# Optimization experiments

Hardware: AMD Instinct MI355X
Metric: run time of the kernel (lower is better)

## Reference

```python
import jax, jax.numpy as jnp
from jax import lax
import numpy as np

IMGSIZE = (360, 640)  # (H, W)
SIGMA = 71.0
LEVEL = 5
FACTOR = 2.0

_k1 = np.array([1., 4., 6., 4., 1.], dtype=np.float32) / 16.0
K5 = np.outer(_k1, _k1)  # 5x5 binomial (Gaussian) pyramid kernel


def _blur(x, scale=1.0):
    # x: (B,C,H,W); depthwise 5x5 Gaussian blur with reflect padding
    C = x.shape[1]
    xp = jnp.pad(x, ((0, 0), (0, 0), (2, 2), (2, 2)), mode='reflect')
    k = jnp.broadcast_to(jnp.asarray(K5 * scale, x.dtype), (C, 1, 5, 5))
    return lax.conv_general_dilated(xp, k, (1, 1), 'VALID',
                                    feature_group_count=C,
                                    dimension_numbers=('NCHW', 'OIHW', 'NCHW'))


def pyrdown(x):
    # OpenCV-style pyrDown: blur then drop every other row/col -> ceil(H/2), ceil(W/2)
    return _blur(x)[:, :, ::2, ::2]


def pyrup(x):
    # OpenCV-style pyrUp: zero-insertion upsample then blur with 4*kernel
    B, C, H, W = x.shape
    up = jnp.zeros((B, C, 2 * H, 2 * W), x.dtype).at[:, :, ::2, ::2].set(x)
    return _blur(up, scale=4.0)


def resize_nearest(x, h, w):
    # matches torch F.interpolate(mode='nearest'): src = floor(dst * in/out)
    H, W = x.shape[-2], x.shape[-1]
    ri = jnp.arange(h) * H // h
    ci = jnp.arange(w) * W // w
    return x[..., ri[:, None], ci[None, :]]


def _create_filter(height, width, sigma):
    s = 2.0 * sigma * sigma
    xc = int(round(width * 0.5))
    yc = int(round(height * 0.5))
    ex = jnp.arange(-xc, width - xc - 1, dtype=jnp.float32)   # (W-1,)
    ey = jnp.arange(-yc, height - yc - 1, dtype=jnp.float32)  # (H-1,)
    d = ex[:, None] ** 2 + ey[None, :] ** 2                   # (W-1, H-1)
    g = jnp.exp(-d / s)
    return (g / g.max()).T                                    # (H-1, W-1)


def _pyramid_filters():
    f = _create_filter(int(FACTOR * IMGSIZE[0]), int(FACTOR * IMGSIZE[1]), SIGMA)
    filters = [f]
    for _ in range(LEVEL):
        filters.append(pyrdown(filters[-1][None, None])[0, 0])
    return filters


def setup_inputs():
    key = jax.random.key(0)
    k1, k2 = jax.random.split(key)
    B, C = 32, 3
    H, W = IMGSIZE
    images = jax.random.normal(k1, (B, C, H, W), jnp.float32)
    u = jax.random.uniform(k2, (B, 2), jnp.float32)
    # fixations are (x, y) pixel coordinates inside the image
    fixations = u * jnp.array([W - 1.0, H - 1.0], jnp.float32)
    return {"images": images, "fixations": fixations}


def reference(images, fixations):
    filters = _pyramid_filters()
    # Laplacian pyramid construction
    pyr, cur = [], images
    up = images
    for _ in range(LEVEL):
        dn = pyrdown(cur)
        up = resize_nearest(pyrup(dn), cur.shape[2], cur.shape[3])
        pyr.append(cur - up)
        cur = dn
    fovea = up  # smallest level, upsampled back (im_smallest)
    for i in range(LEVEL - 1, -1, -1):
        f = filters[i]
        fh, fw = f.shape
        ih, iw = pyr[i].shape[2], pyr[i].shape[3]
        fix = fixations / (2.0 ** i)
        # rect = filter_size/2 - fix, truncated to int (same as torch .to(int64))
        x1 = (fw / 2.0 - fix[:, 0]).astype(jnp.int32)
        y1 = (fh / 2.0 - fix[:, 1]).astype(jnp.int32)
        # per-sample dynamic crop of size (ih, iw); crop size == target size so
        # the original's F.interpolate on the crop is the identity
        crop = jax.vmap(lambda yy, xx: lax.dynamic_slice(f, (yy, xx), (ih, iw)))(y1, x1)
        filtered = pyr[i] * crop[:, None, :, :]
        if i != LEVEL - 1:
            fovea = resize_nearest(pyrup(fovea), ih, iw)
        fovea = fovea + filtered
    return fovea
```

## Files before the change

kernel.cpp:

```cpp
#include <hip/hip_runtime.h>
#include <cstddef>


static __device__ __forceinline__ int refl(int e, int n) {
  if (e < 0) e = -e;
  if (e >= n) e = 2 * n - 2 - e;
  return e;
}

static __device__ __forceinline__ int mapi(int i, int n) {
  return i < 0 ? -i : (i >= n ? n - 1 : i);
}

static __device__ __forceinline__ float4 loadu4(const float* p) {
  float4 v; __builtin_memcpy(&v, p, sizeof(float4)); return v;
}

static __device__ void filt_build(float* pool, float* __restrict__ fyg,
                                  float* __restrict__ fxg) {
  float* sy = pool;
  float* sx = pool + 1394;
  const int oy[5] = {0, 719, 1079, 1259, 1349};
  const int ny[5] = {719, 360, 180, 90, 45};
  const int ox[5] = {0, 1279, 1919, 2239, 2399};
  const int nx[5] = {1279, 640, 320, 160, 80};
  int tid = threadIdx.y * 64 + threadIdx.x;
  for (int i = tid; i < 719; i += 256) {
    float d = (float)(i - 360); sy[i] = expf(-d * d / 10082.0f);
  }
  for (int i = tid; i < 1279; i += 256) {
    float d = (float)(i - 640); sx[i] = expf(-d * d / 10082.0f);
  }
  __syncthreads();
  const float k0 = 0.0625f, k1 = 0.25f, k2 = 0.375f;
#pragma unroll
  for (int l = 1; l < 5; ++l) {
    const float* py = sy + oy[l - 1]; float* qy = sy + oy[l];
    int n = ny[l - 1];
    for (int i = tid; i < ny[l]; i += 256) {
      qy[i] = k0 * (py[refl(2 * i - 2, n)] + py[refl(2 * i + 2, n)]) +
              k1 * (py[refl(2 * i - 1, n)] + py[refl(2 * i + 1, n)]) +
              k2 * py[2 * i];
    }
    const float* px = sx + ox[l - 1]; float* qx = sx + ox[l];
    int m = nx[l - 1];
    for (int i = tid; i < nx[l]; i += 256) {
      qx[i] = k0 * (px[refl(2 * i - 2, m)] + px[refl(2 * i + 2, m)]) +
              k1 * (px[refl(2 * i - 1, m)] + px[refl(2 * i + 1, m)]) +
              k2 * px[2 * i];
    }
    __syncthreads();
  }
  for (int i = tid; i < 1394; i += 256) fyg[i] = sy[i];
  for (int i = tid; i < 2479; i += 256) fxg[i] = sx[i];
}

__global__ __launch_bounds__(256) void pyrdown_lds_k(
    const float* __restrict__ src, float* __restrict__ dst,
    int H, int W, int oH, int oW, int NP,
    float* __restrict__ fyo, float* __restrict__ fxo) {
  __shared__ float pool[35 * 68 * 2];
  int tx = threadIdx.x;
  int ty = threadIdx.y;
  int p  = blockIdx.z;
  if (p >= NP) {
    if (blockIdx.x == 0 && blockIdx.y == 0 && fyo) filt_build(pool, fyo, fxo);
    return;
  }
  float* te = pool;
  float* to_ = pool + 35 * 68;
  int x0 = blockIdx.x * 64;
  int Yb = blockIdx.y;
  const float* s = src + (size_t)p * H * W;
  float* d = dst + (size_t)p * oH * oW;

  int cols = min(64, oW - x0);
  int nq   = (cols + 4) >> 1;
  int gr0  = 32 * Yb - 2;
  int gc0  = 2 * x0 - 4;
  int tid  = ty * 64 + tx;

  auto loadq = [&](int r, int m) -> float4 {
    int gy = refl(gr0 + r, H);
    const float* row = s + (size_t)gy * W;
    int gc = gc0 + 4 * m;
    if (gc >= 0 && gc + 3 < W) return *(const float4*)(row + gc);
    float4 v;
    v.x = row[refl(gc, W)];
    v.y = row[refl(gc + 1, W)];
    v.z = row[refl(gc + 2, W)];
    v.w = row[refl(gc + 3, W)];
    return v;
  };
  auto putq = [&](int r, int m, float4 v) {
    *(float2*)&te[r * 68 + 2 * m]  = make_float2(v.x, v.z);
    *(float2*)&to_[r * 68 + 2 * m] = make_float2(v.y, v.w);
  };

  if (nq == 34) {
    int r0 = tid / 34,          m0 = tid - 34 * r0;
    int q1 = tid + 256;  int r1 = q1 / 34, m1 = q1 - 34 * r1;
    int q2 = tid + 512;  int r2 = q2 / 34, m2 = q2 - 34 * r2;
    int q3 = tid + 768;  int r3 = q3 / 34, m3 = q3 - 34 * r3;
    int q4 = tid + 1024; int r4 = q4 / 34, m4 = q4 - 34 * r4;
    bool g4 = (q4 < 1190);
    float4 v0 = loadq(r0, m0);
    float4 v1 = loadq(r1, m1);
    float4 v2 = loadq(r2, m2);
    float4 v3 = loadq(r3, m3);
    float4 v4;
    if (g4) v4 = loadq(r4, m4);
    putq(r0, m0, v0);
    putq(r1, m1, v1);
    putq(r2, m2, v2);
    putq(r3, m3, v3);
    if (g4) putq(r4, m4, v4);
  } else {
    float4 v[9];
#pragma unroll
    for (int i = 0; i < 9; ++i) {
      int r = ty + 4 * i;
      if (r < 35 && tx < nq) v[i] = loadq(r, tx);
    }
#pragma unroll
    for (int i = 0; i < 9; ++i) {
      int r = ty + 4 * i;
      if (r < 35 && tx < nq) putq(r, tx, v[i]);
    }
  }
  __syncthreads();

  int x = x0 + tx;
  int nPairs = (oH + 1) >> 1;
  int Yp0 = 8 * Yb + 2 * ty;
  if (x < oW && Yp0 < nPairs) {
    const float k0 = 0.0625f, k1 = 0.25f, k2 = 0.375f;
    float h[11];
    int rbase = 8 * ty;
#pragma unroll
    for (int a = 0; a < 11; ++a) {
      int r = rbase + a;
      float e0 = te[r * 68 + tx + 1], e2 = te[r * 68 + tx + 2],
            e4 = te[r * 68 + tx + 3];
      float e1 = to_[r * 68 + tx + 1], e3 = to_[r * 68 + tx + 2];
      h[a] = k0 * (e0 + e4) + k1 * (e1 + e3) + k2 * e2;
    }
    float o0 = k0 * (h[0] + h[4])  + k1 * (h[1] + h[3])  + k2 * h[2];
    float o1 = k0 * (h[2] + h[6])  + k1 * (h[3] + h[5])  + k2 * h[4];
    float o2 = k0 * (h[4] + h[8])  + k1 * (h[5] + h[7])  + k2 * h[6];
    float o3 = k0 * (h[6] + h[10]) + k1 * (h[7] + h[9])  + k2 * h[8];
    int oy0 = 2 * Yp0;
    float* drow = d + (size_t)oy0 * oW + x;
    drow[0] = o0;
    if (oy0 + 1 < oH) drow[(size_t)oW] = o1;
    if (oy0 + 2 < oH) drow[(size_t)2 * oW] = o2;
    if (oy0 + 3 < oH) drow[(size_t)3 * oW] = o3;
  }
}

static __device__ __forceinline__ float pyrdown_at(const float* c, int H, int W,
                                                   int y, int x) {
  const float k0 = 0.0625f, k1 = 0.25f, k2 = 0.375f;
  int c0 = refl(2 * x - 2, W), c1 = refl(2 * x - 1, W), c2 = 2 * x,
      c3 = refl(2 * x + 1, W), c4 = refl(2 * x + 2, W);
  float h[5];
#pragma unroll
  for (int r = 0; r < 5; ++r) {
    int gy = refl(2 * y - 2 + r, H);
    const float* row = c + gy * W;
    h[r] = k0 * (row[c0] + row[c4]) + k1 * (row[c1] + row[c3]) + k2 * row[c2];
  }
  return k0 * (h[0] + h[4]) + k1 * (h[1] + h[3]) + k2 * h[2];
}

static __device__ __forceinline__ float pyrup_at(const float* c, int Hc, int Wc,
                                                 int y, int x) {
  const float w0 = 0.125f, w1 = 0.75f;
  int yc = y >> 1, xc = x >> 1;
  if (y & 1) {
    int yb = (yc == Hc - 1) ? Hc - 1 : yc + 1;
    const float* ra = c + yc * Wc;
    const float* rb = c + yb * Wc;
    if (x & 1) {
      int xb = (xc == Wc - 1) ? Wc - 1 : xc + 1;
      return 0.25f * (ra[xc] + ra[xb] + rb[xc] + rb[xb]);
    } else {
      int xm = (xc == 0) ? 1 : xc - 1, xp = (xc == Wc - 1) ? Wc - 1 : xc + 1;
      float a = w1 * ra[xc] + w0 * (ra[xm] + ra[xp]);
      float b = w1 * rb[xc] + w0 * (rb[xm] + rb[xp]);
      return 0.5f * (a + b);
    }
  } else {
    int ym = (yc == 0) ? 1 : yc - 1, yp = (yc == Hc - 1) ? Hc - 1 : yc + 1;
    const float* rm = c + ym * Wc;
    const float* rc = c + yc * Wc;
    const float* rp = c + yp * Wc;
    if (x & 1) {
      int xb = (xc == Wc - 1) ? Wc - 1 : xc + 1;
      float a = 0.5f * (rm[xc] + rm[xb]);
      float b = 0.5f * (rc[xc] + rc[xb]);
      float e = 0.5f * (rp[xc] + rp[xb]);
      return w1 * b + w0 * (a + e);
    } else {
      int xm = (xc == 0) ? 1 : xc - 1, xp = (xc == Wc - 1) ? Wc - 1 : xc + 1;
      float a = w1 * rm[xc] + w0 * (rm[xm] + rm[xp]);
      float b = w1 * rc[xc] + w0 * (rc[xm] + rc[xp]);
      float e = w1 * rp[xc] + w0 * (rp[xm] + rp[xp]);
      return w1 * b + w0 * (a + e);
    }
  }
}

static __device__ __forceinline__ float pyrup_flat(
    const float* t, int pitch, int yo, int xo, int y, int x) {
  const float w0 = 0.125f, w1 = 0.75f;
  int ys = (y >> 1) - yo, xs = (x >> 1) - xo;
  const float* rc = t + ys * pitch + xs;
  float h0, h1, h2;
  if (x & 1) {
    h1 = 0.5f * (rc[0] + rc[1]);
    h2 = 0.5f * (rc[pitch] + rc[pitch + 1]);
    if (y & 1) return 0.5f * (h1 + h2);
    h0 = 0.5f * (rc[-pitch] + rc[-pitch + 1]);
    return w1 * h1 + w0 * (h0 + h2);
  } else {
    h1 = w1 * rc[0] + w0 * (rc[-1] + rc[1]);
    h2 = w1 * rc[pitch] + w0 * (rc[pitch - 1] + rc[pitch + 1]);
    if (y & 1) return 0.5f * (h1 + h2);
    h0 = w1 * rc[-pitch] + w0 * (rc[-pitch - 1] + rc[-pitch + 1]);
    return w1 * h1 + w0 * (h0 + h2);
  }
}

__global__ __launch_bounds__(256) void tail_k(
    const float* __restrict__ dn3, const float* __restrict__ fix,
    const float* __restrict__ fy3, const float* __restrict__ fx3,
    const float* __restrict__ fy4, const float* __restrict__ fx4,
    float* __restrict__ fv3) {
  __shared__ float c3[45 * 80];
  __shared__ float c4[23 * 40];
  __shared__ float c5[12 * 20];
  __shared__ float g4[23 * 40];
  int p = blockIdx.x;
  int tid = threadIdx.x;
  const float* src = dn3 + (size_t)p * 3600;
  for (int i = tid; i < 900; i += 256)
    ((float4*)c3)[i] = ((const float4*)src)[i];
  __syncthreads();
  for (int i = tid; i < 23 * 40; i += 256) {
    int y = i / 40, x = i - 40 * y;
    c4[i] = pyrdown_at(c3, 45, 80, y, x);
  }
  __syncthreads();
  for (int i = tid; i < 12 * 20; i += 256) {
    int y = i / 20, x = i - 20 * y;
    c5[i] = pyrdown_at(c4, 23, 40, y, x);
  }
  __syncthreads();
  int b = p / 3;
  float fxv = fix[2 * b + 0], fyv = fix[2 * b + 1];
  {
    int x1 = (int)(40.0f - fxv * 0.0625f);
    int y1 = (int)(22.5f - fyv * 0.0625f);
    for (int i = tid; i < 23 * 40; i += 256) {
      int y = i / 40, x = i - 40 * y;
      float u = pyrup_at(c5, 12, 20, y, x);
      g4[i] = u + (c4[i] - u) * (fy4[y1 + y] * fx4[x1 + x]);
    }
  }
  __syncthreads();
  {
    int x1 = (int)(80.0f - fxv * 0.125f);
    int y1 = (int)(45.0f - fyv * 0.125f);
    float* dst = fv3 + (size_t)p * 3600;
    for (int i = tid; i < 45 * 80; i += 256) {
      int y = i / 80, x = i - 80 * y;
      float uf = pyrup_at(g4, 23, 40, y, x);
      float ud = pyrup_at(c4, 23, 40, y, x);
      dst[i] = uf + (c3[i] - ud) * (fy3[y1 + y] * fx3[x1 + x]);
    }
  }
}

__global__ __launch_bounds__(256) void recon_fused_k(
    const float* __restrict__ images, const float* __restrict__ dn1,
    const float* __restrict__ dn2, const float* __restrict__ dn3,
    const float* __restrict__ fv3g, const float* __restrict__ fyg,
    const float* __restrict__ fxg, const float* __restrict__ fix,
    float* __restrict__ out) {
  __shared__ float fv1t[10 * 67];
  __shared__ float dn1t[10 * 67];
  __shared__ float fv2t[7 * 35];
  __shared__ float dn2t[7 * 35];
  __shared__ float fv3t[5 * 19];
  __shared__ float dn3t[5 * 19];
  const int bx = blockIdx.x, by = blockIdx.y, p = blockIdx.z;
  const int tid = threadIdx.x;
  const int R1o = 8 * by - 1, C1o = 64 * bx - 1;
  const int R2o = 4 * by - 1, C2o = 32 * bx - 1;
  const int R3o = 2 * by - 1, C3o = 16 * bx - 1;
  const float* d1p = dn1 + (size_t)p * 57600;
  const float* d2p = dn2 + (size_t)p * 14400;
  const float* d3p = dn3 + (size_t)p * 3600;
  const float* f3p = fv3g + (size_t)p * 3600;

  for (int s = tid; s < 660; s += 256) {
    int r = s / 66, c = s - 66 * r;
    int gy = mapi(R1o + r, 180), gx = mapi(C1o + c, 320);
    dn1t[r * 67 + c] = d1p[gy * 320 + gx];
  }
  if (tid < 245) {
    int r = tid / 35, c = tid - 35 * r;
    int gy = mapi(R2o + r, 90), gx = mapi(C2o + c, 160);
    dn2t[tid] = d2p[gy * 160 + gx];
  }
  if (tid < 95) {
    int r = tid / 19, c = tid - 19 * r;
    int gy = mapi(R3o + r, 45), gx = mapi(C3o + c, 80);
    dn3t[tid] = d3p[gy * 80 + gx];
    fv3t[tid] = f3p[gy * 80 + gx];
  }
  __syncthreads();

  int b = p / 3;
  float fxv = fix[2 * b + 0], fyv = fix[2 * b + 1];
  int y1_2 = (int)(90.0f - fyv * 0.25f), x1_2 = (int)(160.0f - fxv * 0.25f);
  int y1_1 = (int)(180.0f - fyv * 0.5f), x1_1 = (int)(320.0f - fxv * 0.5f);
  int y1_0 = (int)(359.5f - fyv),        x1_0 = (int)(639.5f - fxv);
  const float* fy2 = fyg + 1079; const float* fx2 = fxg + 1919;
  const float* fy1 = fyg + 719;  const float* fx1 = fxg + 1279;

  if (tid < 245) {
    int r = tid / 35, c = tid - 35 * r;
    int gy = mapi(R2o + r, 90), gx = mapi(C2o + c, 160);
    float uf = pyrup_flat(fv3t, 19, R3o, C3o, gy, gx);
    float ud = pyrup_flat(dn3t, 19, R3o, C3o, gy, gx);
    fv2t[tid] = uf + (dn2t[tid] - ud) * (fy2[y1_2 + gy] * fx2[x1_2 + gx]);
  }
  __syncthreads();

  for (int s = tid; s < 660; s += 256) {
    int r = s / 66, c = s - 66 * r;
    int gy = mapi(R1o + r, 180), gx = mapi(C1o + c, 320);
    float uf = pyrup_flat(fv2t, 35, R2o, C2o, gy, gx);
    float ud = pyrup_flat(dn2t, 35, R2o, C2o, gy, gx);
    fv1t[r * 67 + c] =
        uf + (dn1t[r * 67 + c] - ud) * (fy1[y1_1 + gy] * fx1[x1_1 + gx]);
  }
  __syncthreads();

  int trow = tid >> 5;
  int tk   = tid & 31;
  int Y = 8 * by + trow;
  if (Y >= 180) return;
  int c0 = 64 * bx + 2 * tk;
  const float* dbase = dn1t + trow * 67 + 2 * tk;
  const float* ebase = fv1t + trow * 67 + 2 * tk;
  float dm[3], da[3], db[3], dq[3], em[3], ea[3], eb[3], eq[3];
#pragma unroll
  for (int r = 0; r < 3; ++r) {
    const float* q = dbase + r * 67;
    dm[r] = q[0]; da[r] = q[1]; db[r] = q[2]; dq[r] = q[3];
    const float* e = ebase + r * 67;
    em[r] = e[0]; ea[r] = e[1]; eb[r] = e[2]; eq[r] = e[3];
  }

  const float w0 = 0.125f, w1 = 0.75f;
  float heA[3], hoA[3], heB[3], hoB[3];
#pragma unroll
  for (int r = 0; r < 3; ++r) {
    heA[r] = w1 * da[r] + w0 * (dm[r] + db[r]);
    hoA[r] = 0.5f * (da[r] + db[r]);
    heB[r] = w1 * db[r] + w0 * (da[r] + dq[r]);
    hoB[r] = 0.5f * (db[r] + dq[r]);
  }
  float u00 = w1 * heA[1] + w0 * (heA[0] + heA[2]);
  float u01 = w1 * hoA[1] + w0 * (hoA[0] + hoA[2]);
  float u02 = w1 * heB[1] + w0 * (heB[0] + heB[2]);
  float u03 = w1 * hoB[1] + w0 * (hoB[0] + hoB[2]);
  float u10 = 0.5f * (heA[1] + heA[2]);
  float u11 = 0.5f * (hoA[1] + hoA[2]);
  float u12 = 0.5f * (heB[1] + heB[2]);
  float u13 = 0.5f * (hoB[1] + hoB[2]);

  float geA[3], goA[3], geB[3], goB[3];
#pragma unroll
  for (int r = 0; r < 3; ++r) {
    geA[r] = w1 * ea[r] + w0 * (em[r] + eb[r]);
    goA[r] = 0.5f * (ea[r] + eb[r]);
    geB[r] = w1 * eb[r] + w0 * (ea[r] + eq[r]);
    goB[r] = 0.5f * (eb[r] + eq[r]);
  }
  float f00 = w1 * geA[1] + w0 * (geA[0] + geA[2]);
  float f01 = w1 * goA[1] + w0 * (goA[0] + goA[2]);
  float f02 = w1 * geB[1] + w0 * (geB[0] + geB[2]);
  float f03 = w1 * goB[1] + w0 * (goB[0] + goB[2]);
  float f10 = 0.5f * (geA[1] + geA[2]);
  float f11 = 0.5f * (goA[1] + goA[2]);
  float f12 = 0.5f * (geB[1] + geB[2]);
  float f13 = 0.5f * (goB[1] + goB[2]);

  int oy = 2 * Y, ox = 2 * c0;
  const float* crow = images + (size_t)p * 230400 + (size_t)oy * 640 + ox;
  float* orow = out + (size_t)p * 230400 + (size_t)oy * 640 + ox;
  float fyA = fyg[y1_0 + oy], fyB = fyg[y1_0 + oy + 1];
  float4 fxq = loadu4(fxg + (x1_0 + ox));

  float4 cv = *(const float4*)crow;
  float4 r0v;
  r0v.x = f00 + (cv.x - u00) * (fyA * fxq.x);
  r0v.y = f01 + (cv.y - u01) * (fyA * fxq.y);
  r0v.z = f02 + (cv.z - u02) * (fyA * fxq.z);
  r0v.w = f03 + (cv.w - u03) * (fyA * fxq.w);
  *(float4*)orow = r0v;
  float4 cv1 = *(const float4*)(crow + 640);
  float4 r1v;
  r1v.x = f10 + (cv1.x - u10) * (fyB * fxq.x);
  r1v.y = f11 + (cv1.y - u11) * (fyB * fxq.y);
  r1v.z = f12 + (cv1.z - u12) * (fyB * fxq.z);
  r1v.w = f13 + (cv1.w - u13) * (fyB * fxq.w);
  *(float4*)(orow + 640) = r1v;
}

extern "C" void kernel_launch(void* const* d_in, const int* in_sizes, int n_in,
                              void* d_out, int out_size, void* d_ws, size_t ws_size,
                              hipStream_t stream) {
  const float* images = (const float*)d_in[0];
  const float* fix    = (const float*)d_in[1];
  float* out = (float*)d_out;
  float* ws  = (float*)d_ws;

  const int P = 96;

  size_t off = 0;
  auto alloc = [&](size_t n) { float* p = ws + off; off += (n + 3) & ~(size_t)3; return p; };
  float* fyg = alloc(1394);
  float* fxg = alloc(2479);
  float* dn1 = alloc((size_t)P * 180 * 320);
  float* dn2 = alloc((size_t)P * 90 * 160);
  float* dn3 = alloc((size_t)P * 45 * 80);
  float* fv3 = alloc((size_t)P * 45 * 80);
  if (ws_size < off * sizeof(float)) return;

  dim3 blk(64, 4, 1);
  auto pgrd = [](int oW, int oH, int p) {
    int nPairs = (oH + 1) / 2;
    return dim3((unsigned)((oW + 63) / 64), (unsigned)((nPairs + 7) / 8), (unsigned)p);
  };

  pyrdown_lds_k<<<pgrd(320, 180, P + 1), blk, 0, stream>>>(
      images, dn1, 360, 640, 180, 320, P, fyg, fxg);
  pyrdown_lds_k<<<pgrd(160, 90, P), blk, 0, stream>>>(
      dn1, dn2, 180, 320, 90, 160, P, nullptr, nullptr);
  pyrdown_lds_k<<<pgrd(80, 45, P), blk, 0, stream>>>(
      dn2, dn3, 90, 160, 45, 80, P, nullptr, nullptr);

  tail_k<<<dim3(P), dim3(256), 0, stream>>>(
      dn3, fix, fyg + 1259, fxg + 2239, fyg + 1349, fxg + 2399, fv3);

  recon_fused_k<<<dim3(5, 23, P), dim3(256), 0, stream>>>(
      images, dn1, dn2, dn3, fv3, fyg, fxg, fix, out);
}
```

Before: 233.3 us.

## Compute pyramid reconstruction per coarse cell producing 2x2 outputs, drop halo duplication

The fused reconstruction kernel now stages only the in-range tile rows and columns instead of mirrored halos. Each thread computes the shared horizontal and vertical pyrUp partial sums once per coarse cell and emits all four fine outputs, rather than recomputing the full stencil per output pixel. Border reflection moves into index arithmetic at use time. This removes redundant separable-filter arithmetic and per-pixel parity branching in the level-3 to level-2 and level-2 to level-1 stages, at the cost of more complex index bookkeeping and bounds checks.

```diff
diff --git a/kernel.cpp b/kernel.cpp
--- a/kernel.cpp
+++ b/kernel.cpp
@@ -6,10 +6,6 @@
   if (e < 0) e = -e;
   if (e >= n) e = 2 * n - 2 - e;
   return e;
-}
-
-static __device__ __forceinline__ int mapi(int i, int n) {
-  return i < 0 ? -i : (i >= n ? n - 1 : i);
 }
 
 static __device__ __forceinline__ float4 loadu4(const float* p) {
@@ -211,27 +207,6 @@
   }
 }
 
-static __device__ __forceinline__ float pyrup_flat(
-    const float* t, int pitch, int yo, int xo, int y, int x) {
-  const float w0 = 0.125f, w1 = 0.75f;
-  int ys = (y >> 1) - yo, xs = (x >> 1) - xo;
-  const float* rc = t + ys * pitch + xs;
-  float h0, h1, h2;
-  if (x & 1) {
-    h1 = 0.5f * (rc[0] + rc[1]);
-    h2 = 0.5f * (rc[pitch] + rc[pitch + 1]);
-    if (y & 1) return 0.5f * (h1 + h2);
-    h0 = 0.5f * (rc[-pitch] + rc[-pitch + 1]);
-    return w1 * h1 + w0 * (h0 + h2);
-  } else {
-    h1 = w1 * rc[0] + w0 * (rc[-1] + rc[1]);
-    h2 = w1 * rc[pitch] + w0 * (rc[pitch - 1] + rc[pitch + 1]);
-    if (y & 1) return 0.5f * (h1 + h2);
-    h0 = w1 * rc[-pitch] + w0 * (rc[-pitch - 1] + rc[-pitch + 1]);
-    return w1 * h1 + w0 * (h0 + h2);
-  }
-}
-
 __global__ __launch_bounds__(256) void tail_k(
     const float* __restrict__ dn3, const float* __restrict__ fix,
     const float* __restrict__ fy3, const float* __restrict__ fx3,
@@ -288,37 +263,48 @@
     const float* __restrict__ fv3g, const float* __restrict__ fyg,
     const float* __restrict__ fxg, const float* __restrict__ fix,
     float* __restrict__ out) {
-  __shared__ float fv1t[10 * 67];
-  __shared__ float dn1t[10 * 67];
-  __shared__ float fv2t[7 * 35];
-  __shared__ float dn2t[7 * 35];
-  __shared__ float fv3t[5 * 19];
-  __shared__ float dn3t[5 * 19];
+  __shared__ float dn1t[670], fv1t[670];
+  __shared__ float dn2t[296], fv2t[296];
+  __shared__ float dn3t[126], fv3t[126];
   const int bx = blockIdx.x, by = blockIdx.y, p = blockIdx.z;
   const int tid = threadIdx.x;
-  const int R1o = 8 * by - 1, C1o = 64 * bx - 1;
-  const int R2o = 4 * by - 1, C2o = 32 * bx - 1;
-  const int R3o = 2 * by - 1, C3o = 16 * bx - 1;
+
+  const int R1r = max(8 * by - 1, 0),  R1hi = min(8 * by + 8, 179);
+  const int C1r = max(64 * bx - 1, 0), C1hi = min(64 * bx + 64, 319);
+  const int n1r = R1hi - R1r + 1, n1c = C1hi - C1r + 1;
+  const int yc_lo = R1r >> 1, yc_hi = R1hi >> 1;
+  const int xc_lo = C1r >> 1, xc_hi = C1hi >> 1;
+  const int R2r = max(yc_lo - 1, 0),  R2hi = min(yc_hi + 1, 89);
+  const int C2r = max(xc_lo - 1, 0),  C2hi = min(xc_hi + 1, 159);
+  const int n2r = R2hi - R2r + 1, n2c = C2hi - C2r + 1;
+  const int yc3_lo = R2r >> 1, yc3_hi = R2hi >> 1;
+  const int xc3_lo = C2r >> 1, xc3_hi = C2hi >> 1;
+  const int R3r = max(yc3_lo - 1, 0), R3hi = min(yc3_hi + 1, 44);
+  const int C3r = max(xc3_lo - 1, 0), C3hi = min(xc3_hi + 1, 79);
+  const int n3r = R3hi - R3r + 1, n3c = C3hi - C3r + 1;
+
   const float* d1p = dn1 + (size_t)p * 57600;
   const float* d2p = dn2 + (size_t)p * 14400;
   const float* d3p = dn3 + (size_t)p * 3600;
   const float* f3p = fv3g + (size_t)p * 3600;
 
-  for (int s = tid; s < 660; s += 256) {
-    int r = s / 66, c = s - 66 * r;
-    int gy = mapi(R1o + r, 180), gx = mapi(C1o + c, 320);
-    dn1t[r * 67 + c] = d1p[gy * 320 + gx];
-  }
-  if (tid < 245) {
-    int r = tid / 35, c = tid - 35 * r;
-    int gy = mapi(R2o + r, 90), gx = mapi(C2o + c, 160);
-    dn2t[tid] = d2p[gy * 160 + gx];
-  }
-  if (tid < 95) {
-    int r = tid / 19, c = tid - 19 * r;
-    int gy = mapi(R3o + r, 45), gx = mapi(C3o + c, 80);
-    dn3t[tid] = d3p[gy * 80 + gx];
-    fv3t[tid] = f3p[gy * 80 + gx];
+  for (int s = tid; s < 670; s += 256) {
+    int r = s / 67, c = s - 67 * r;
+    if (r < n1r && c < n1c)
+      dn1t[s] = d1p[(R1r + r) * 320 + (C1r + c)];
+  }
+  for (int s = tid; s < 296; s += 256) {
+    int r = s / 37, c = s - 37 * r;
+    if (r < n2r && c < n2c)
+      dn2t[s] = d2p[(R2r + r) * 160 + (C2r + c)];
+  }
+  if (tid < 126) {
+    int r = tid / 21, c = tid - 21 * r;
+    if (r < n3r && c < n3c) {
+      int o = (R3r + r) * 80 + (C3r + c);
+      dn3t[tid] = d3p[o];
+      fv3t[tid] = f3p[o];
+    }
   }
   __syncthreads();
 
@@ -329,23 +315,99 @@
   int y1_0 = (int)(359.5f - fyv),        x1_0 = (int)(639.5f - fxv);
   const float* fy2 = fyg + 1079; const float* fx2 = fxg + 1919;
   const float* fy1 = fyg + 719;  const float* fx1 = fxg + 1279;
-
-  if (tid < 245) {
-    int r = tid / 35, c = tid - 35 * r;
-    int gy = mapi(R2o + r, 90), gx = mapi(C2o + c, 160);
-    float uf = pyrup_flat(fv3t, 19, R3o, C3o, gy, gx);
-    float ud = pyrup_flat(dn3t, 19, R3o, C3o, gy, gx);
-    fv2t[tid] = uf + (dn2t[tid] - ud) * (fy2[y1_2 + gy] * fx2[x1_2 + gx]);
-  }
-  __syncthreads();
-
-  for (int s = tid; s < 660; s += 256) {
-    int r = s / 66, c = s - 66 * r;
-    int gy = mapi(R1o + r, 180), gx = mapi(C1o + c, 320);
-    float uf = pyrup_flat(fv2t, 35, R2o, C2o, gy, gx);
-    float ud = pyrup_flat(dn2t, 35, R2o, C2o, gy, gx);
-    fv1t[r * 67 + c] =
-        uf + (dn1t[r * 67 + c] - ud) * (fy1[y1_1 + gy] * fx1[x1_1 + gx]);
+  const float w0 = 0.125f, w1 = 0.75f;
+
+  {
+    int nx3 = xc3_hi - xc3_lo + 1;
+    int ncell = (yc3_hi - yc3_lo + 1) * nx3;
+    if (tid < ncell) {
+      int cy = tid / nx3;
+      int yc = yc3_lo + cy, xc = xc3_lo + (tid - cy * nx3);
+      int aa0 = ((yc == 0) ? 1 : yc - 1) - R3r;
+      int aa1 = yc - R3r;
+      int aa2 = ((yc == 44) ? 44 : yc + 1) - R3r;
+      int xm = ((xc == 0) ? 1 : xc - 1) - C3r;
+      int xq = xc - C3r;
+      int xp = ((xc == 79) ? 79 : xc + 1) - C3r;
+      int aa[3] = {aa0, aa1, aa2};
+      float heF[3], hoF[3], heD[3], hoD[3];
+#pragma unroll
+      for (int j = 0; j < 3; ++j) {
+        const float* rf = fv3t + aa[j] * 21;
+        float fm = rf[xm], fc = rf[xq], fp = rf[xp];
+        heF[j] = w1 * fc + w0 * (fm + fp);
+        hoF[j] = 0.5f * (fc + fp);
+        const float* rd = dn3t + aa[j] * 21;
+        float em = rd[xm], ec = rd[xq], ep = rd[xp];
+        heD[j] = w1 * ec + w0 * (em + ep);
+        hoD[j] = 0.5f * (ec + ep);
+      }
+      float uF[4] = {w1 * heF[1] + w0 * (heF[0] + heF[2]),
+                     w1 * hoF[1] + w0 * (hoF[0] + hoF[2]),
+                     0.5f * (heF[1] + heF[2]),
+                     0.5f * (hoF[1] + hoF[2])};
+      float uD[4] = {w1 * heD[1] + w0 * (heD[0] + heD[2]),
+                     w1 * hoD[1] + w0 * (hoD[0] + hoD[2]),
+                     0.5f * (heD[1] + heD[2]),
+                     0.5f * (hoD[1] + hoD[2])};
+      int y2 = 2 * yc, x2 = 2 * xc;
+#pragma unroll
+      for (int q = 0; q < 4; ++q) {
+        int y = y2 + (q >> 1), x = x2 + (q & 1);
+        if (y >= R2r && y <= R2hi && x >= C2r && x <= C2hi) {
+          int idx = (y - R2r) * 37 + (x - C2r);
+          float w = fy2[y1_2 + y] * fx2[x1_2 + x];
+          fv2t[idx] = uF[q] + (dn2t[idx] - uD[q]) * w;
+        }
+      }
+    }
+  }
+  __syncthreads();
+
+  {
+    int nx2 = xc_hi - xc_lo + 1;
+    int ncell = (yc_hi - yc_lo + 1) * nx2;
+    if (tid < ncell) {
+      int cy = tid / nx2;
+      int yc = yc_lo + cy, xc = xc_lo + (tid - cy * nx2);
+      int aa0 = ((yc == 0) ? 1 : yc - 1) - R2r;
+      int aa1 = yc - R2r;
+      int aa2 = ((yc == 89) ? 89 : yc + 1) - R2r;
+      int xm = ((xc == 0) ? 1 : xc - 1) - C2r;
+      int xq = xc - C2r;
+      int xp = ((xc == 159) ? 159 : xc + 1) - C2r;
+      int aa[3] = {aa0, aa1, aa2};
+      float heF[3], hoF[3], heD[3], hoD[3];
+#pragma unroll
+      for (int j = 0; j < 3; ++j) {
+        const float* rf = fv2t + aa[j] * 37;
+        float fm = rf[xm], fc = rf[xq], fp = rf[xp];
+        heF[j] = w1 * fc + w0 * (fm + fp);
+        hoF[j] = 0.5f * (fc + fp);
+        const float* rd = dn2t + aa[j] * 37;
+        float em = rd[xm], ec = rd[xq], ep = rd[xp];
+        heD[j] = w1 * ec + w0 * (em + ep);
+        hoD[j] = 0.5f * (ec + ep);
+      }
+      float uF[4] = {w1 * heF[1] + w0 * (heF[0] + heF[2]),
+                     w1 * hoF[1] + w0 * (hoF[0] + hoF[2]),
+                     0.5f * (heF[1] + heF[2]),
+                     0.5f * (hoF[1] + hoF[2])};
+      float uD[4] = {w1 * heD[1] + w0 * (heD[0] + heD[2]),
+                     w1 * hoD[1] + w0 * (hoD[0] + hoD[2]),
+                     0.5f * (heD[1] + heD[2]),
+                     0.5f * (hoD[1] + hoD[2])};
+      int y2 = 2 * yc, x2 = 2 * xc;
+#pragma unroll
+      for (int q = 0; q < 4; ++q) {
+        int y = y2 + (q >> 1), x = x2 + (q & 1);
+        if (y >= R1r && y <= R1hi && x >= C1r && x <= C1hi) {
+          int idx = (y - R1r) * 67 + (x - C1r);
+          float w = fy1[y1_1 + y] * fx1[x1_1 + x];
+          fv1t[idx] = uF[q] + (dn1t[idx] - uD[q]) * w;
+        }
+      }
+    }
   }
   __syncthreads();
 
@@ -354,18 +416,23 @@
   int Y = 8 * by + trow;
   if (Y >= 180) return;
   int c0 = 64 * bx + 2 * tk;
-  const float* dbase = dn1t + trow * 67 + 2 * tk;
-  const float* ebase = fv1t + trow * 67 + 2 * tk;
+  int ry[3];
+  ry[0] = ((Y == 0) ? 1 : Y - 1) - R1r;
+  ry[1] = Y - R1r;
+  ry[2] = ((Y == 179) ? 179 : Y + 1) - R1r;
+  int cm = ((c0 == 0) ? 1 : c0 - 1) - C1r;
+  int cc = c0 - C1r;
+  int cp = ((c0 + 2 >= 320) ? 319 : c0 + 2) - C1r;
+
   float dm[3], da[3], db[3], dq[3], em[3], ea[3], eb[3], eq[3];
 #pragma unroll
   for (int r = 0; r < 3; ++r) {
-    const float* q = dbase + r * 67;
-    dm[r] = q[0]; da[r] = q[1]; db[r] = q[2]; dq[r] = q[3];
-    const float* e = ebase + r * 67;
-    em[r] = e[0]; ea[r] = e[1]; eb[r] = e[2]; eq[r] = e[3];
-  }
-
-  const float w0 = 0.125f, w1 = 0.75f;
+    const float* qd = dn1t + ry[r] * 67;
+    dm[r] = qd[cm]; da[r] = qd[cc]; db[r] = qd[cc + 1]; dq[r] = qd[cp];
+    const float* qe = fv1t + ry[r] * 67;
+    em[r] = qe[cm]; ea[r] = qe[cc]; eb[r] = qe[cc + 1]; eq[r] = qe[cp];
+  }
+
   float heA[3], hoA[3], heB[3], hoB[3];
 #pragma unroll
   for (int r = 0; r < 3; ++r) {
```

Measured after the change: 231.7 us. No clear change (-0.7%).
